# Performance work log

Measured on AMD Instinct MI355X. Metric: run time of the kernel, lower is better.

The kernel has to match this reference:

```python
import jax, jax.numpy as jnp
import numpy as np

N_QUBITS = 8
INPUT_DIM = 128
HIDDEN = 8
T = 512
B = 512


def _build_circuit_consts(n):
    # wire 0 is the most-significant bit of the 2^n basis index (torchquantum layout)
    dim = 1 << n
    idx = np.arange(dim)
    bits = (idx[:, None] >> (n - 1 - np.arange(n))) & 1          # [dim, n]
    zsign = (1 - 2 * bits).astype(np.float32)                     # <Z_w> signs, [dim, n]
    # compose CNOT(0,1)...CNOT(n-2,n-1), CNOT(n-1,0) into one permutation
    perm = idx.copy()
    pairs = [(i, i + 1) for i in range(n - 1)] + [(n - 1, 0)]
    for c, t in pairs:
        cmask = 1 << (n - 1 - c)
        tmask = 1 << (n - 1 - t)
        g = np.where(idx & cmask, idx ^ tmask, idx)               # flip target bit if control set
        perm = perm[g]
    return jnp.asarray(perm), jnp.asarray(zsign)

_PERM, _ZSIGN = _build_circuit_consts(N_QUBITS)


def _qlayer(z, theta):
    # RX(x) then RX(theta) on |0> per wire -> product state; CNOT ring permutes the
    # basis amplitudes, so probabilities permute; MeasureAll(PauliZ) = probs @ zsign.
    a = 0.5 * (z + theta[None, :])                                # [B, n]
    pq = jnp.stack([jnp.cos(a) ** 2, jnp.sin(a) ** 2], axis=-1)   # [B, n, 2]
    probs = pq[:, 0, :]
    for w in range(1, N_QUBITS):                                  # small fixed kron loop
        probs = (probs[:, :, None] * pq[:, w, None, :]).reshape(probs.shape[0], -1)
    probs = probs[:, _PERM]                                       # CNOT ring
    return probs @ _ZSIGN                                         # [B, n] expvals in [-1, 1]


def setup_inputs() -> dict:
    key = jax.random.key(0)
    ks = jax.random.split(key, 14)
    d_in = INPUT_DIM + HIDDEN
    mk_w = lambda k: jax.random.normal(k, (d_in, N_QUBITS), dtype=jnp.float32) * 0.05
    mk_t = lambda k: jax.random.normal(k, (N_QUBITS,), dtype=jnp.float32) * 0.1
    return {
        "inputs": jax.random.normal(ks[0], (T, B, INPUT_DIM), dtype=jnp.float32),
        "Wf": mk_w(ks[1]), "bf": jnp.zeros((N_QUBITS,), jnp.float32),
        "Wi": mk_w(ks[2]), "bi": jnp.zeros((N_QUBITS,), jnp.float32),
        "Wu": mk_w(ks[3]), "bu": jnp.zeros((N_QUBITS,), jnp.float32),
        "Wo": mk_w(ks[4]), "bo": jnp.zeros((N_QUBITS,), jnp.float32),
        "theta_f": mk_t(ks[5]), "theta_i": mk_t(ks[6]),
        "theta_u": mk_t(ks[7]), "theta_o": mk_t(ks[8]),
    }


def reference(inputs, Wf, bf, Wi, bi, Wu, bu, Wo, bo,
              theta_f, theta_i, theta_u, theta_o):
    hx0 = jnp.zeros((inputs.shape[1], HIDDEN), inputs.dtype)
    cx0 = jnp.zeros((inputs.shape[1], HIDDEN), inputs.dtype)

    def step(carry, x):
        hx, cx = carry
        comb = jnp.concatenate([x, hx], axis=1)                   # [B, D+H]
        f = jax.nn.sigmoid(_qlayer(comb @ Wf + bf, theta_f))
        i = jax.nn.sigmoid(_qlayer(comb @ Wi + bi, theta_i))
        g = jnp.tanh(_qlayer(comb @ Wu + bu, theta_u))
        o = jax.nn.sigmoid(_qlayer(comb @ Wo + bo, theta_o))
        cx = f * cx + i * g
        hx = o * jnp.tanh(cx)
        return (hx, cx), hx

    (hx, cx), outputs = jax.lax.scan(step, (hx0, cx0), inputs)
    return outputs, hx, cx
```

## Files before the change

kernel.cpp:

```cpp
#include <hip/hip_runtime.h>
#include <stdint.h>

#define T_STEPS 512
#define BATCH   512
#define IN_DIM  128
#define GDIM    32
#define SLICE   (BATCH * GDIM)
#define INV2PI  0.15915494309189535f

typedef float f4 __attribute__((ext_vector_type(4)));

template <int CTRL>
__device__ __forceinline__ float dppm(float x) {
    return __int_as_float(__builtin_amdgcn_mov_dpp(__float_as_int(x), CTRL, 0xF, 0xF, true));
}
template <int CTRL>
__device__ __forceinline__ float dppk(float old, float x) {
    return __int_as_float(__builtin_amdgcn_update_dpp(
        __float_as_int(old), __float_as_int(x), CTRL, 0xF, 0xF, false));
}

__device__ __forceinline__ float tanh_pade(float x) {
    float u = x * x;
    float n = fmaf(u, u + 105.0f, 945.0f);
    float d = fmaf(u, fmaf(u, 15.0f, 420.0f), 945.0f);
    return (x * n) * __builtin_amdgcn_rcpf(d);
}

__device__ __forceinline__ void gload_lds16(const float* g, float* l) {
    __builtin_amdgcn_global_load_lds(
        (const __attribute__((address_space(1))) void*)g,
        (__attribute__((address_space(3))) void*)l, 16, 0, 0);
}

__global__ __launch_bounds__(256) void qlstm_xproj(
    const float* __restrict__ inp,
    const float* __restrict__ Wf, const float* __restrict__ bf,
    const float* __restrict__ Wi, const float* __restrict__ bi,
    const float* __restrict__ Wu, const float* __restrict__ bu,
    const float* __restrict__ Wo, const float* __restrict__ bo,
    const float* __restrict__ thf, const float* __restrict__ thi,
    const float* __restrict__ thu, const float* __restrict__ tho,
    float* __restrict__ X)
{
    __shared__ float tile[64 * 130];
    const int tid = threadIdx.x;
    const long long row0 = (long long)blockIdx.x * 64;

    const f4* src = (const f4*)(inp + row0 * IN_DIM);
    #pragma unroll
    for (int i = 0; i < 8; ++i) {
        int f = tid + i * 256;
        f4 v = __builtin_nontemporal_load(src + f);
        int r = f >> 5, c = (f & 31) << 2;
        float* d = &tile[r * 130 + c];
        d[0] = v.x; d[1] = v.y; d[2] = v.z; d[3] = v.w;
    }
    __syncthreads();

    const int g  = __builtin_amdgcn_readfirstlane(tid >> 6);
    const int rl = tid & 63;

    const float* W  = (g == 0) ? Wf : (g == 1) ? Wi : (g == 2) ? Wu : Wo;
    const float* B  = (g == 0) ? bf : (g == 1) ? bi : (g == 2) ? bu : bo;
    const float* TH = (g == 0) ? thf : (g == 1) ? thi : (g == 2) ? thu : tho;

    float acc[8];
    #pragma unroll
    for (int j = 0; j < 8; ++j) acc[j] = B[j] + TH[j];

    const float2* trow = (const float2*)&tile[rl * 130];
    #pragma unroll 8
    for (int k2 = 0; k2 < 64; ++k2) {
        float2 v = trow[k2];
        int k = 2 * k2;
        #pragma unroll
        for (int j = 0; j < 8; ++j) {
            acc[j] = fmaf(v.x, W[k * 8 + j], acc[j]);
            acc[j] = fmaf(v.y, W[(k + 1) * 8 + j], acc[j]);
        }
    }

    float4* Xo = (float4*)(X + (row0 + rl) * GDIM + g * 8);
    Xo[0] = make_float4(acc[0] * INV2PI, acc[1] * INV2PI, acc[2] * INV2PI, acc[3] * INV2PI);
    Xo[1] = make_float4(acc[4] * INV2PI, acc[5] * INV2PI, acc[6] * INV2PI, acc[7] * INV2PI);
}

__global__ __launch_bounds__(64, 1) void qlstm_rec(
    const float* __restrict__ X,
    const float* __restrict__ Wf, const float* __restrict__ Wi,
    const float* __restrict__ Wu, const float* __restrict__ Wo,
    float* __restrict__ out)
{
    __shared__ float xb[2 * 2 * 128 * 32];

    const int lane = threadIdx.x;
    const int p    = lane & 15;
    const int q    = p >> 1;
    const int par  = lane & 1;
    const int s    = lane >> 5;
    const int bb   = (lane >> 4) & 1;
    const int qd   = (lane >> 2) & 3;
    const int gate = s * 2 + par;
    const int b    = blockIdx.x * 2 + bb;
    const int col  = s * 16 + par * 8 + q;

    const bool isq0   = (q == 0);
    const bool loHalf = (lane < 32);
    const bool sB     = (s == 1);
    const bool parB   = (par == 1);

    const float* Wg = (gate == 0) ? Wf : (gate == 1) ? Wi : (gate == 2) ? Wu : Wo;
    float wv[8];
    #pragma unroll
    for (int i = 0; i < 8; ++i)
        wv[i] = Wg[(IN_DIM + (i ^ (qd << 1))) * 8 + q] * INV2PI;

    const bool  isT = (gate == 2);
    const float G0 = isT ? 0.9999014f  : 0.24997535f;
    const float G1 = isT ? -0.3310474f : -0.02069046f;
    const float G2 = isT ? 0.1204402f  : 0.00188188f;
    const float G3 = isT ? -0.0277f    : -0.000108203f;
    const float bbv = isT ? 0.0f : 0.5f;

    const float* g0 = X + (lane >> 3) * SLICE + (lane & 7) * 4
                        + blockIdx.x * 2 * GDIM;
    auto stage = [&](int bi, int qs) {
        #pragma unroll
        for (int j = 0; j < 2; ++j) {
            float* dst = &xb[(bi * 2 + j) * 4096];
            const float* srcb = g0 + j * GDIM + qs * SLICE;
            #pragma unroll
            for (int n = 0; n < 16; ++n)
                gload_lds16(srcb + n * 8 * SLICE, dst + n * 256);
        }
    };

    stage(0, 0);
    asm volatile("s_waitcnt vmcnt(0)" ::: "memory");

    const float* xq0 = &xb[bb * 4096 + col];
    float xv0 = xq0[0];
    float xv1 = xq0[32];
    stage(1, 128);

    float hx = 0.0f, cx = 0.0f;
    const float ONE = 1.0f;
    float* outp = out + b * 8 + q;

    for (int qt = 0; qt < 4; ++qt) {
        const int bi = qt & 1;
        const float* xq = &xb[bi * 8192 + bb * 4096 + col];
        if (qt > 0) {
            asm volatile("s_waitcnt vmcnt(0)" ::: "memory");
            xv0 = xq[0];
            xv1 = xq[32];
            if (qt < 3) stage(1 - bi, (qt + 1) * 128);
        }

        auto qstep = [&](int t, int ls, float& XV) {
            float xv = XV;
            XV = xq[((ls + 2) & 127) * 32];

            float Ba = dppm<0x00>(hx);
            float Bb = dppm<0xAA>(hx);
            float Bc = dppm<0x141>(Ba);
            float Bd = dppm<0x141>(Bb);
            float Be = dppm<0x140>(Ba);
            float Bf = dppm<0x140>(Bb);
            float Bg = dppm<0x128>(Ba);
            float Bk = dppm<0x128>(Bb);

            float A1 = fmaf(Bb, wv[1], fmaf(Ba, wv[0], xv));
            float A2 = fmaf(Bd, wv[3], Bc * wv[2]);
            float A3 = fmaf(Bf, wv[7], Be * wv[6]);
            float A4 = fmaf(Bk, wv[5], Bg * wv[4]);
            float z  = (A1 + A2) + (A3 + A4);

            float cq = __builtin_amdgcn_cosf(z);

            float cc  = fabsf(cq) < 1e-30f ? 1e-30f : cq;
            float rcpc = __builtin_amdgcn_rcpf(cc);

            float P = cq * dppk<0x112>(ONE, cq);
            P = P * dppk<0x114>(ONE, P);
            P = P * dppk<0x118>(ONE, P);

            float Pfull = dppm<0x10E>(P);
            float out0  = Pfull * rcpc;
            float outv  = isq0 ? out0 : P;

            float u  = outv * outv;
            float u2 = u * u;
            float t1 = fmaf(u, G1, G0);
            float t2 = fmaf(u, G3, G2);
            float G  = fmaf(u2, t2, t1);
            float act = fmaf(outv, G, bbv);

            float n1 = dppm<0xB1>(act);
            auto pr = __builtin_amdgcn_permlane32_swap(
                __float_as_int(act), __float_as_int(act), false, false);
            float sw = __int_as_float(loHalf ? pr[1] : pr[0]);
            float sw2 = dppm<0xB1>(sw);

            float X1 = parB ? n1  : act;
            float X2 = parB ? act : n1;
            float Y1 = parB ? sw2 : sw;
            float Y2 = parB ? sw  : sw2;

            float fv = sB ? Y1 : X1;
            float iv = sB ? Y2 : X2;
            float uv = sB ? X1 : Y1;
            float ov = sB ? X2 : Y2;

            float ncx = fmaf(fv, cx, iv * uv);
            float nhx = ov * tanh_pade(ncx);
            cx = ncx;
            hx = nhx;

            __builtin_nontemporal_store(nhx, outp + t * (BATCH * 8));
        };

        #pragma unroll 2
        for (int ls = 0; ls < 128; ls += 2) {
            qstep(qt * 128 + ls,     ls,     xv0);
            qstep(qt * 128 + ls + 1, ls + 1, xv1);
        }
    }

    __builtin_nontemporal_store(hx, out + T_STEPS * BATCH * 8 + b * 8 + q);
    __builtin_nontemporal_store(cx, out + T_STEPS * BATCH * 8 + (BATCH + b) * 8 + q);
}

extern "C" void kernel_launch(void* const* d_in, const int* in_sizes, int n_in,
                              void* d_out, int out_size, void* d_ws, size_t ws_size,
                              hipStream_t stream) {
    const float* inp = (const float*)d_in[0];
    const float* Wf  = (const float*)d_in[1];
    const float* bf  = (const float*)d_in[2];
    const float* Wi  = (const float*)d_in[3];
    const float* bi  = (const float*)d_in[4];
    const float* Wu  = (const float*)d_in[5];
    const float* bu  = (const float*)d_in[6];
    const float* Wo  = (const float*)d_in[7];
    const float* bo  = (const float*)d_in[8];
    const float* thf = (const float*)d_in[9];
    const float* thi = (const float*)d_in[10];
    const float* thu = (const float*)d_in[11];
    const float* tho = (const float*)d_in[12];

    float* X   = (float*)d_ws;
    float* out = (float*)d_out;

    qlstm_xproj<<<(T_STEPS * BATCH) / 64, 256, 0, stream>>>(
        inp, Wf, bf, Wi, bi, Wu, bu, Wo, bo, thf, thi, thu, tho, X);

    qlstm_rec<<<BATCH / 2, 64, 0, stream>>>(X, Wf, Wi, Wu, Wo, out);
}
```

Baseline: 128.8 us.

## Warp-specialize xproj with producer/consumer double-buffered LDS tiles

The input projection kernel now uses 512-thread blocks. Half the threads are producers that stream the next 64-row input tile into a second LDS buffer, while the other half compute the gate projections on the current tile. Each block handles 8 tiles in sequence, so the grid shrinks by a factor of eight. The goal is to overlap global loads with the FMA work, at the cost of fewer blocks, twice the LDS per block, and a barrier per tile.

```diff
diff --git a/kernel.cpp b/kernel.cpp
--- a/kernel.cpp
+++ b/kernel.cpp
@@ -33,7 +33,7 @@
         (__attribute__((address_space(3))) void*)l, 16, 0, 0);
 }
 
-__global__ __launch_bounds__(256) void qlstm_xproj(
+__global__ __launch_bounds__(512) void qlstm_xproj(
     const float* __restrict__ inp,
     const float* __restrict__ Wf, const float* __restrict__ bf,
     const float* __restrict__ Wi, const float* __restrict__ bi,
@@ -43,47 +43,76 @@
     const float* __restrict__ thu, const float* __restrict__ tho,
     float* __restrict__ X)
 {
-    __shared__ float tile[64 * 130];
+    __shared__ float tile[2][64 * 130];
     const int tid = threadIdx.x;
-    const long long row0 = (long long)blockIdx.x * 64;
-
-    const f4* src = (const f4*)(inp + row0 * IN_DIM);
-    #pragma unroll
-    for (int i = 0; i < 8; ++i) {
-        int f = tid + i * 256;
-        f4 v = __builtin_nontemporal_load(src + f);
-        int r = f >> 5, c = (f & 31) << 2;
-        float* d = &tile[r * 130 + c];
-        d[0] = v.x; d[1] = v.y; d[2] = v.z; d[3] = v.w;
+    const int t0  = blockIdx.x * 8;
+    const bool producer = (tid < 256);
+
+    if (producer) {
+        const f4* src = (const f4*)(inp + (long long)t0 * 64 * IN_DIM);
+        #pragma unroll
+        for (int j = 0; j < 8; ++j) {
+            int f = tid + j * 256;
+            f4 v = __builtin_nontemporal_load(src + f);
+            int r = f >> 5, c = (f & 31) << 2;
+            float* d = &tile[0][r * 130 + c];
+            d[0] = v.x; d[1] = v.y; d[2] = v.z; d[3] = v.w;
+        }
     }
-    __syncthreads();
-
-    const int g  = __builtin_amdgcn_readfirstlane(tid >> 6);
-    const int rl = tid & 63;
-
+
+    const int c0 = tid - 256;
+    const int g  = __builtin_amdgcn_readfirstlane(c0 >> 6) & 3;
+    const int rl = c0 & 63;
     const float* W  = (g == 0) ? Wf : (g == 1) ? Wi : (g == 2) ? Wu : Wo;
     const float* B  = (g == 0) ? bf : (g == 1) ? bi : (g == 2) ? bu : bo;
     const float* TH = (g == 0) ? thf : (g == 1) ? thi : (g == 2) ? thu : tho;
-
-    float acc[8];
+    float binit[8];
     #pragma unroll
-    for (int j = 0; j < 8; ++j) acc[j] = B[j] + TH[j];
-
-    const float2* trow = (const float2*)&tile[rl * 130];
-    #pragma unroll 8
-    for (int k2 = 0; k2 < 64; ++k2) {
-        float2 v = trow[k2];
-        int k = 2 * k2;
-        #pragma unroll
-        for (int j = 0; j < 8; ++j) {
-            acc[j] = fmaf(v.x, W[k * 8 + j], acc[j]);
-            acc[j] = fmaf(v.y, W[(k + 1) * 8 + j], acc[j]);
-        }
+    for (int j = 0; j < 8; ++j) binit[j] = B[j] + TH[j];
+
+    __syncthreads();
+
+    for (int i = 0; i < 8; ++i) {
+        if (producer) {
+            if (i < 7) {
+                const f4* src = (const f4*)(inp + (long long)(t0 + i + 1) * 64 * IN_DIM);
+                f4 v[8];
+                #pragma unroll
+                for (int j = 0; j < 8; ++j)
+                    v[j] = __builtin_nontemporal_load(src + tid + j * 256);
+                float* buf = tile[(i + 1) & 1];
+                #pragma unroll
+                for (int j = 0; j < 8; ++j) {
+                    int f = tid + j * 256;
+                    int r = f >> 5, c = (f & 31) << 2;
+                    float* d = &buf[r * 130 + c];
+                    d[0] = v[j].x; d[1] = v[j].y; d[2] = v[j].z; d[3] = v[j].w;
+                }
+            }
+        } else {
+            float acc[8];
+            #pragma unroll
+            for (int j = 0; j < 8; ++j) acc[j] = binit[j];
+
+            const float2* trow = (const float2*)&tile[i & 1][rl * 130];
+            #pragma unroll 8
+            for (int k2 = 0; k2 < 64; ++k2) {
+                float2 v = trow[k2];
+                int k = 2 * k2;
+                #pragma unroll
+                for (int j = 0; j < 8; ++j) {
+                    acc[j] = fmaf(v.x, W[k * 8 + j], acc[j]);
+                    acc[j] = fmaf(v.y, W[(k + 1) * 8 + j], acc[j]);
+                }
+            }
+
+            long long row0 = (long long)(t0 + i) * 64;
+            float4* Xo = (float4*)(X + (row0 + rl) * GDIM + g * 8);
+            Xo[0] = make_float4(acc[0] * INV2PI, acc[1] * INV2PI, acc[2] * INV2PI, acc[3] * INV2PI);
+            Xo[1] = make_float4(acc[4] * INV2PI, acc[5] * INV2PI, acc[6] * INV2PI, acc[7] * INV2PI);
+        }
+        __syncthreads();
     }
-
-    float4* Xo = (float4*)(X + (row0 + rl) * GDIM + g * 8);
-    Xo[0] = make_float4(acc[0] * INV2PI, acc[1] * INV2PI, acc[2] * INV2PI, acc[3] * INV2PI);
-    Xo[1] = make_float4(acc[4] * INV2PI, acc[5] * INV2PI, acc[6] * INV2PI, acc[7] * INV2PI);
 }
 
 __global__ __launch_bounds__(64, 1) void qlstm_rec(
@@ -252,7 +281,7 @@
     float* X   = (float*)d_ws;
     float* out = (float*)d_out;
 
-    qlstm_xproj<<<(T_STEPS * BATCH) / 64, 256, 0, stream>>>(
+    qlstm_xproj<<<(T_STEPS * BATCH) / (64 * 8), 512, 0, stream>>>(
         inp, Wf, bf, Wi, bi, Wu, bu, Wo, bo, thf, thi, thu, tho, X);
 
     qlstm_rec<<<BATCH / 2, 64, 0, stream>>>(X, Wf, Wi, Wu, Wo, out);
```

Result: faster. 125.5 us, median of 2 (-2.6%).
